# Kernel optimization log

Hardware: AMD Instinct MI355X
Metric: run time of the kernel (lower is better)

## Reference

```python
import jax, jax.numpy as jnp
import numpy as np

CROP_H = 7
CROP_W = 7
EXTRAP = 0.0  # module hardcodes 0 when calling CropAndResizeFunction


def _crop_and_resize(image, boxes, box_ind):
    """TF-style crop_and_resize.
    image: (N,C,H,W) float; boxes: (M,4) normalized (y1,x1,y2,x2); box_ind: (M,) int32.
    Returns (M,C,CROP_H,CROP_W).
    """
    N, C, H, W = image.shape
    dt = image.dtype
    y1, x1, y2, x2 = boxes[:, 0], boxes[:, 1], boxes[:, 2], boxes[:, 3]
    ii = jnp.arange(CROP_H, dtype=dt)
    jj = jnp.arange(CROP_W, dtype=dt)
    # sample coordinates in feature-map space, shape (M, CROP_H) / (M, CROP_W)
    y = y1[:, None] * (H - 1) + ii[None, :] * ((y2 - y1) * (H - 1) / (CROP_H - 1))[:, None]
    x = x1[:, None] * (W - 1) + jj[None, :] * ((x2 - x1) * (W - 1) / (CROP_W - 1))[:, None]
    valid_y = (y >= 0) & (y <= H - 1)
    valid_x = (x >= 0) & (x <= W - 1)
    yt_f = jnp.floor(y)
    xt_f = jnp.floor(x)
    y_lerp = y - yt_f  # (M, oh)
    x_lerp = x - xt_f  # (M, ow)
    yt = jnp.clip(yt_f, 0, H - 1).astype(jnp.int32)
    yb = jnp.clip(jnp.ceil(y), 0, H - 1).astype(jnp.int32)
    xl = jnp.clip(xt_f, 0, W - 1).astype(jnp.int32)
    xr = jnp.clip(jnp.ceil(x), 0, W - 1).astype(jnp.int32)
    img = jnp.transpose(image, (0, 2, 3, 1))  # (N,H,W,C) for clean gather
    b = box_ind[:, None, None]                # (M,1,1)
    tl = img[b, yt[:, :, None], xl[:, None, :]]  # (M,oh,ow,C)
    tr = img[b, yt[:, :, None], xr[:, None, :]]
    bl = img[b, yb[:, :, None], xl[:, None, :]]
    br = img[b, yb[:, :, None], xr[:, None, :]]
    xl_w = x_lerp[:, None, :, None]
    top = tl + (tr - tl) * xl_w
    bot = bl + (br - bl) * xl_w
    out = top + (bot - top) * y_lerp[:, :, None, None]
    valid = (valid_y[:, :, None] & valid_x[:, None, :])[..., None]
    out = jnp.where(valid, out, jnp.asarray(EXTRAP, dt))
    return jnp.transpose(out, (0, 3, 1, 2))  # (M,C,oh,ow)


def setup_inputs() -> dict:
    key = jax.random.key(0)
    k0, k1, k2, k3, k4, k5 = jax.random.split(key, 6)
    N, C, H, W = 2, 256, 200, 304
    M = 2048
    scale = 0.0625  # 1/16
    Himg, Wimg = H / scale, W / scale
    featuremap = jax.random.normal(k0, (N, C, H, W), dtype=jnp.float32)
    x1 = jax.random.uniform(k1, (M, 1), minval=0.0, maxval=Wimg - 260.0)
    y1 = jax.random.uniform(k2, (M, 1), minval=0.0, maxval=Himg - 260.0)
    bw = jax.random.uniform(k3, (M, 1), minval=32.0, maxval=256.0)
    bh = jax.random.uniform(k4, (M, 1), minval=32.0, maxval=256.0)
    ids = jax.random.randint(k5, (M, 1), 0, N).astype(jnp.float32)
    rois = jnp.concatenate([ids, x1, y1, x1 + bw, y1 + bh], axis=1)
    return {"featuremap": featuremap, "rois": rois, "spatial_scale": jnp.float32(scale)}


def reference(featuremap, rois, spatial_scale):
    H, W = featuremap.shape[2], featuremap.shape[3]
    boxes = rois[:, 1:5] * spatial_scale
    box_ind = rois[:, 0].astype(jnp.int32)
    x1, y1, x2, y2 = boxes[:, 0], boxes[:, 1], boxes[:, 2], boxes[:, 3]
    spacing_w = (x2 - x1) / CROP_W
    spacing_h = (y2 - y1) / CROP_H
    nx0 = (x1 + spacing_w / 2 - 0.5) / (W - 1)
    ny0 = (y1 + spacing_h / 2 - 0.5) / (H - 1)
    nw = spacing_w * (CROP_W - 1) / (W - 1)
    nh = spacing_h * (CROP_H - 1) / (H - 1)
    boxes_n = jnp.stack([ny0, nx0, ny0 + nh, nx0 + nw], axis=1)
    return _crop_and_resize(featuremap, boxes_n, box_ind)
```

## Files before the change

kernel.cpp:

```cpp
#include <hip/hip_runtime.h>

#define RA_C   256
#define RA_H   200
#define RA_W   304
#define RA_HW  (RA_H * RA_W)
#define RA_CHW (RA_C * RA_HW)
#define CROPN  7
#define CROP2  (CROPN * CROPN)
#define OUT_M  (RA_C * CROP2)
#define BC     8
#define BB     2
#define REG_R  16
#define REG_C  20
#define NF4    5
#define CH_STR (REG_R * REG_C + 4)
#define GREC   64

__global__ __launch_bounds__(256) void geom_kernel(
    const float* __restrict__ rois, const float* __restrict__ scale_p,
    int* __restrict__ ws, int M)
{
    const int gid = blockIdx.x * 256 + threadIdx.x;
    if (gid >= M * 2 * CROPN) return;
    {
        #pragma clang fp contract(off)
        const int m   = gid / (2 * CROPN);
        const int k14 = gid - m * (2 * CROPN);
        int* __restrict__ rec = ws + (size_t)m * GREC;
        const int axis = (k14 >= CROPN) ? 1 : 0;
        const int k = axis ? (k14 - CROPN) : k14;
        const float scale = scale_p[0];
        const float* __restrict__ rr = rois + (size_t)m * 5;
        float lo, hi, szm1;
        if (axis == 0) { lo = rr[2] * scale; hi = rr[4] * scale; szm1 = (float)(RA_H - 1); }
        else           { lo = rr[1] * scale; hi = rr[3] * scale; szm1 = (float)(RA_W - 1); }
        float sp   = (hi - lo) / 7.0f;
        float n0   = (lo + sp * 0.5f - 0.5f) / szm1;
        float nsz  = sp * 6.0f / szm1;
        float b2   = n0 + nsz;
        float d    = (b2 - n0) * szm1 / 6.0f;
        float coord = n0 * szm1 + (float)k * d;
        float fl = floorf(coord);
        float ce = ceilf(coord);
        float lerp = coord - fl;
        int lo_i = (int)fminf(fmaxf(fl, 0.0f), szm1);
        int hi_i = (int)fminf(fmaxf(ce, 0.0f), szm1);
        float valid = (coord >= 0.0f && coord <= szm1) ? 1.0f : 0.0f;
        if (axis == 0) {
            rec[k]      = lo_i;
            rec[7 + k]  = hi_i;
            rec[28 + k] = __float_as_int(lerp);
            rec[35 + k] = __float_as_int(valid);
            if (k == 0) {
                rec[56] = lo_i;
                rec[58] = (int)rr[0] * RA_CHW;
            }
        } else {
            rec[14 + k] = lo_i;
            rec[21 + k] = hi_i;
            rec[42 + k] = __float_as_int(lerp);
            rec[49 + k] = __float_as_int(valid);
            if (k == 0) rec[57] = lo_i & ~3;
        }
    }
}

__global__ __launch_bounds__(256) void roialign_kernel(
    const float* __restrict__ fm, const int* __restrict__ ws,
    float* __restrict__ out)
{
    __shared__ __align__(16) float s_reg[BB * BC * CH_STR];
    __shared__ int s_tab[BB][GREC];

    const int t = threadIdx.x;

    const int bid   = blockIdx.x;
    const int numBG = gridDim.x >> 5;
    const int xcd   = bid & 7;
    const int r     = bid >> 3;
    const int cgl   = r / numBG;
    const int bg    = r - cgl * numBG;
    const int m0    = bg * BB;
    const int c0    = (xcd * 4 + cgl) * BC;

    const int bx = t >> 7;
    const int* __restrict__ rec = ws + (size_t)(m0 + bx) * GREC;

    const int ys   = rec[56];
    const int xs   = rec[57];
    const int base = rec[58] + c0 * RA_HW;

    const int u   = t & 127;
    const int cc  = u >> 4;
    const int l16 = u & 15;
    const float* __restrict__ cp = fm + (size_t)(base + cc * RA_HW);
    float4 v[NF4];
    #pragma unroll
    for (int s = 0; s < NF4; ++s) {
        const int idx = l16 + (s << 4);
        const int r2  = idx / 5;
        const int kk  = idx - r2 * 5;
        const int row = min(ys + r2, RA_H - 1);
        const int col = min(xs + (kk << 2), RA_W - 4);
        v[s] = *reinterpret_cast<const float4*>(cp + row * RA_W + col);
    }

    if (t < BB * GREC) {
        const int b = t >> 6;
        const int w = t & 63;
        s_tab[b][w] = ws[(size_t)(m0 + b) * GREC + w];
    }

    {
        float* __restrict__ sp_ = s_reg + (bx * BC + cc) * CH_STR;
        #pragma unroll
        for (int s = 0; s < NF4; ++s) {
            const int idx = l16 + (s << 4);
            *reinterpret_cast<float4*>(sp_ + (idx << 2)) = v[s];
        }
    }
    __syncthreads();

    const int ij  = t & 63;
    const int chg = (t >> 6) & 1;
    if (ij < CROP2) {
        const int i = ij / CROPN;
        const int j = ij - i * CROPN;
        const int rT = min(s_tab[bx][i]      - ys, REG_R - 1);
        const int rB = min(s_tab[bx][7 + i]  - ys, REG_R - 1);
        const int cl = min(s_tab[bx][14 + j] - xs, REG_C - 1);
        const int cr = min(s_tab[bx][21 + j] - xs, REG_C - 1);
        const float yw = __int_as_float(s_tab[bx][28 + i]);
        const float vy = __int_as_float(s_tab[bx][35 + i]);
        const float xw = __int_as_float(s_tab[bx][42 + j]);
        const float vx = __int_as_float(s_tab[bx][49 + j]);
        const float vv = vy * vx;
        const int oT = rT * REG_C;
        const int oB = rB * REG_C;
        float* __restrict__ op =
            out + (size_t)(m0 + bx) * OUT_M + (size_t)(c0 + chg * 4) * CROP2 + ij;
        #pragma unroll
        for (int q = 0; q < 4; ++q) {
            const float* __restrict__ sp2 =
                s_reg + (bx * BC + chg * 4 + q) * CH_STR;
            const float tl = sp2[oT + cl];
            const float tr = sp2[oT + cr];
            const float bl = sp2[oB + cl];
            const float br = sp2[oB + cr];
            const float top = tl + (tr - tl) * xw;
            const float bot = bl + (br - bl) * xw;
            op[q * CROP2] = (top + (bot - top) * yw) * vv;
        }
    }
}

extern "C" void kernel_launch(void* const* d_in, const int* in_sizes, int n_in,
                              void* d_out, int out_size, void* d_ws, size_t ws_size,
                              hipStream_t stream) {
    const float* fm    = (const float*)d_in[0];
    const float* rois  = (const float*)d_in[1];
    const float* scale = (const float*)d_in[2];
    float* out = (float*)d_out;
    int* ws = (int*)d_ws;
    const int M = in_sizes[1] / 5;
    const int numBG = M / BB;

    const int gthreads = M * 2 * CROPN;
    geom_kernel<<<dim3((gthreads + 255) / 256), dim3(256), 0, stream>>>(
        rois, scale, ws, M);
    roialign_kernel<<<dim3(32 * numBG), dim3(256), 0, stream>>>(fm, ws, out);
}
```

Before: 273.6 us.

## Make roialign blocks persistent over four box pairs with register-prefetch pipelining

Each block now handles four consecutive box pairs instead of one. While interpolating the current pair from shared memory, it prefetches the next pair's feature-map region into registers and the geometry table into a double-buffered shared table. This cuts the grid by a factor of four and hides global-load latency behind the interpolation. The cost is two barriers per iteration, more register pressure, and fewer blocks to fill the GPU.

Result: slower. 423.8 us (+54.9%).

```diff
diff --git a/kernel.cpp b/kernel.cpp
--- a/kernel.cpp
+++ b/kernel.cpp
@@ -15,6 +15,8 @@
 #define NF4    5
 #define CH_STR (REG_R * REG_C + 4)
 #define GREC   64
+#define PREC   (BB * GREC)
+#define NITER  4
 
 __global__ __launch_bounds__(256) void geom_kernel(
     const float* __restrict__ rois, const float* __restrict__ scale_p,
@@ -70,48 +72,49 @@
     float* __restrict__ out)
 {
     __shared__ __align__(16) float s_reg[BB * BC * CH_STR];
-    __shared__ int s_tab[BB][GREC];
+    __shared__ int s_tab[2][PREC];
 
     const int t = threadIdx.x;
 
-    const int bid   = blockIdx.x;
-    const int numBG = gridDim.x >> 5;
-    const int xcd   = bid & 7;
-    const int r     = bid >> 3;
-    const int cgl   = r / numBG;
-    const int bg    = r - cgl * numBG;
-    const int m0    = bg * BB;
-    const int c0    = (xcd * 4 + cgl) * BC;
-
-    const int bx = t >> 7;
-    const int* __restrict__ rec = ws + (size_t)(m0 + bx) * GREC;
-
-    const int ys   = rec[56];
-    const int xs   = rec[57];
-    const int base = rec[58] + c0 * RA_HW;
-
+    const int bid    = blockIdx.x;
+    const int numBlk = gridDim.x >> 5;
+    const int xcd    = bid & 7;
+    const int r      = bid >> 3;
+    const int cgl    = r / numBlk;
+    const int bgrp   = r - cgl * numBlk;
+    const int c0     = (xcd * 4 + cgl) * BC;
+    const int mp0    = bgrp * NITER;
+
+    const int bx  = t >> 7;
     const int u   = t & 127;
     const int cc  = u >> 4;
     const int l16 = u & 15;
-    const float* __restrict__ cp = fm + (size_t)(base + cc * RA_HW);
-    float4 v[NF4];
-    #pragma unroll
-    for (int s = 0; s < NF4; ++s) {
-        const int idx = l16 + (s << 4);
-        const int r2  = idx / 5;
-        const int kk  = idx - r2 * 5;
-        const int row = min(ys + r2, RA_H - 1);
-        const int col = min(xs + (kk << 2), RA_W - 4);
-        v[s] = *reinterpret_cast<const float4*>(cp + row * RA_W + col);
-    }
-
-    if (t < BB * GREC) {
-        const int b = t >> 6;
-        const int w = t & 63;
-        s_tab[b][w] = ws[(size_t)(m0 + b) * GREC + w];
-    }
-
+
+    const int ij  = t & 63;
+    const int chg = (t >> 6) & 1;
+    const int si  = ij / CROPN;
+    const int sj  = ij - si * CROPN;
+
+    if (t < PREC) {
+        s_tab[0][t] = ws[(size_t)mp0 * PREC + t];
+        s_tab[1][t] = ws[(size_t)(mp0 + 1) * PREC + t];
+    }
     {
+        const int* __restrict__ rec0 = ws + (size_t)(mp0 * BB + bx) * GREC;
+        const int ys0   = rec0[56];
+        const int xs0   = rec0[57];
+        const int base0 = rec0[58] + c0 * RA_HW;
+        const float* __restrict__ cp0 = fm + (size_t)(base0 + cc * RA_HW);
+        float4 v[NF4];
+        #pragma unroll
+        for (int s = 0; s < NF4; ++s) {
+            const int idx = l16 + (s << 4);
+            const int r2  = idx / 5;
+            const int kk  = idx - r2 * 5;
+            const int row = min(ys0 + r2, RA_H - 1);
+            const int col = min(xs0 + (kk << 2), RA_W - 4);
+            v[s] = *reinterpret_cast<const float4*>(cp0 + row * RA_W + col);
+        }
         float* __restrict__ sp_ = s_reg + (bx * BC + cc) * CH_STR;
         #pragma unroll
         for (int s = 0; s < NF4; ++s) {
@@ -121,36 +124,76 @@
     }
     __syncthreads();
 
-    const int ij  = t & 63;
-    const int chg = (t >> 6) & 1;
-    if (ij < CROP2) {
-        const int i = ij / CROPN;
-        const int j = ij - i * CROPN;
-        const int rT = min(s_tab[bx][i]      - ys, REG_R - 1);
-        const int rB = min(s_tab[bx][7 + i]  - ys, REG_R - 1);
-        const int cl = min(s_tab[bx][14 + j] - xs, REG_C - 1);
-        const int cr = min(s_tab[bx][21 + j] - xs, REG_C - 1);
-        const float yw = __int_as_float(s_tab[bx][28 + i]);
-        const float vy = __int_as_float(s_tab[bx][35 + i]);
-        const float xw = __int_as_float(s_tab[bx][42 + j]);
-        const float vx = __int_as_float(s_tab[bx][49 + j]);
-        const float vv = vy * vx;
-        const int oT = rT * REG_C;
-        const int oB = rB * REG_C;
-        float* __restrict__ op =
-            out + (size_t)(m0 + bx) * OUT_M + (size_t)(c0 + chg * 4) * CROP2 + ij;
-        #pragma unroll
-        for (int q = 0; q < 4; ++q) {
-            const float* __restrict__ sp2 =
-                s_reg + (bx * BC + chg * 4 + q) * CH_STR;
-            const float tl = sp2[oT + cl];
-            const float tr = sp2[oT + cr];
-            const float bl = sp2[oB + cl];
-            const float br = sp2[oB + cr];
-            const float top = tl + (tr - tl) * xw;
-            const float bot = bl + (br - bl) * xw;
-            op[q * CROP2] = (top + (bot - top) * yw) * vv;
-        }
+    #pragma unroll
+    for (int it = 0; it < NITER; ++it) {
+        const int cur = it & 1;
+        const int nxt = cur ^ 1;
+
+        float4 vn[NF4];
+        if (it + 1 < NITER) {
+            const int* __restrict__ tbn = s_tab[nxt] + bx * GREC;
+            const int ysn   = tbn[56];
+            const int xsn   = tbn[57];
+            const int basen = tbn[58] + c0 * RA_HW;
+            const float* __restrict__ cpn = fm + (size_t)(basen + cc * RA_HW);
+            #pragma unroll
+            for (int s = 0; s < NF4; ++s) {
+                const int idx = l16 + (s << 4);
+                const int r2  = idx / 5;
+                const int kk  = idx - r2 * 5;
+                const int row = min(ysn + r2, RA_H - 1);
+                const int col = min(xsn + (kk << 2), RA_W - 4);
+                vn[s] = *reinterpret_cast<const float4*>(cpn + row * RA_W + col);
+            }
+        }
+        int rw = 0;
+        if (it + 2 < NITER && t < PREC)
+            rw = ws[(size_t)(mp0 + it + 2) * PREC + t];
+
+        if (ij < CROP2) {
+            const int* __restrict__ tb = s_tab[cur] + bx * GREC;
+            const int ysc = tb[56];
+            const int xsc = tb[57];
+            const int rT = min(tb[si]      - ysc, REG_R - 1);
+            const int rB = min(tb[7 + si]  - ysc, REG_R - 1);
+            const int cl = min(tb[14 + sj] - xsc, REG_C - 1);
+            const int cr = min(tb[21 + sj] - xsc, REG_C - 1);
+            const float yw = __int_as_float(tb[28 + si]);
+            const float vy = __int_as_float(tb[35 + si]);
+            const float xw = __int_as_float(tb[42 + sj]);
+            const float vx = __int_as_float(tb[49 + sj]);
+            const float vv = vy * vx;
+            const int oT = rT * REG_C;
+            const int oB = rB * REG_C;
+            const int m  = (mp0 + it) * BB + bx;
+            float* __restrict__ op =
+                out + (size_t)m * OUT_M + (size_t)(c0 + chg * 4) * CROP2 + ij;
+            #pragma unroll
+            for (int q = 0; q < 4; ++q) {
+                const float* __restrict__ sp2 =
+                    s_reg + (bx * BC + chg * 4 + q) * CH_STR;
+                const float tl = sp2[oT + cl];
+                const float tr = sp2[oT + cr];
+                const float bl = sp2[oB + cl];
+                const float br = sp2[oB + cr];
+                const float top = tl + (tr - tl) * xw;
+                const float bot = bl + (br - bl) * xw;
+                op[q * CROP2] = (top + (bot - top) * yw) * vv;
+            }
+        }
+        __syncthreads();
+
+        if (it + 1 < NITER) {
+            float* __restrict__ sp_ = s_reg + (bx * BC + cc) * CH_STR;
+            #pragma unroll
+            for (int s = 0; s < NF4; ++s) {
+                const int idx = l16 + (s << 4);
+                *reinterpret_cast<float4*>(sp_ + (idx << 2)) = vn[s];
+            }
+            if (it + 2 < NITER && t < PREC)
+                s_tab[cur][t] = rw;
+        }
+        __syncthreads();
     }
 }
 
@@ -163,10 +206,10 @@
     float* out = (float*)d_out;
     int* ws = (int*)d_ws;
     const int M = in_sizes[1] / 5;
-    const int numBG = M / BB;
+    const int numBlk = (M / BB) / NITER;
 
     const int gthreads = M * 2 * CROPN;
     geom_kernel<<<dim3((gthreads + 255) / 256), dim3(256), 0, stream>>>(
         rois, scale, ws, M);
-    roialign_kernel<<<dim3(32 * numBG), dim3(256), 0, stream>>>(fm, ws, out);
+    roialign_kernel<<<dim3(32 * numBlk), dim3(256), 0, stream>>>(fm, ws, out);
 }
```

## Sort ROIs by batch and spatial position before the gather kernel

Applied to the files above, without the earlier changes.

Adds a single-block bitonic sort kernel that orders ROI geometry records by (batch index, top row, left column) and copies them into a second workspace buffer. The gather kernel then processes spatially neighbouring ROIs in adjacent blocks and writes each result to the ROI's original output slot. The intent is better L2/MALL reuse of feature-map reads across overlapping ROIs. In exchange it adds an extra serial launch that runs on a single block, and the sorted path only runs when M is 2048 and the workspace is large enough.

New measurement: 348.9 us. 1.28x slower.

```diff
diff --git a/kernel.cpp b/kernel.cpp
--- a/kernel.cpp
+++ b/kernel.cpp
@@ -54,6 +54,7 @@
             if (k == 0) {
                 rec[56] = lo_i;
                 rec[58] = (int)rr[0] * RA_CHW;
+                rec[59] = m;
             }
         } else {
             rec[14 + k] = lo_i;
@@ -65,8 +66,43 @@
     }
 }
 
+__global__ __launch_bounds__(1024) void sort_kernel(int* __restrict__ ws, int M)
+{
+    __shared__ unsigned s_k[2048];
+    const int t = threadIdx.x;
+    for (int i = t; i < M; i += 1024) {
+        const int* __restrict__ rec = ws + (size_t)i * GREC;
+        const unsigned b  = rec[58] ? 1u : 0u;
+        const unsigned ys = (unsigned)rec[56] & 0xFFu;
+        const unsigned xs = (unsigned)rec[57] & 0x1FFu;
+        s_k[i] = (b << 28) | (ys << 20) | (xs << 11) | (unsigned)i;
+    }
+    __syncthreads();
+    for (unsigned k = 2; k <= 2048; k <<= 1) {
+        for (unsigned j = k >> 1; j > 0; j >>= 1) {
+            for (unsigned i = t; i < 2048; i += 1024) {
+                const unsigned ixj = i ^ j;
+                if (ixj > i) {
+                    const unsigned a = s_k[i], c = s_k[ixj];
+                    const bool descending = ((i & k) != 0);
+                    if ((a > c) != descending) { s_k[i] = c; s_k[ixj] = a; }
+                }
+            }
+            __syncthreads();
+        }
+    }
+    int* __restrict__ dst = ws + (size_t)M * GREC;
+    const int total = M * GREC;
+    for (int w = t; w < total; w += 1024) {
+        const int p    = w >> 6;
+        const int word = w & 63;
+        const int src  = (int)(s_k[p] & 0x7FFu);
+        dst[w] = ws[(size_t)src * GREC + word];
+    }
+}
+
 __global__ __launch_bounds__(256) void roialign_kernel(
-    const float* __restrict__ fm, const int* __restrict__ ws,
+    const float* __restrict__ fm, const int* __restrict__ recs,
     float* __restrict__ out)
 {
     __shared__ __align__(16) float s_reg[BB * BC * CH_STR];
@@ -84,7 +120,7 @@
     const int c0    = (xcd * 4 + cgl) * BC;
 
     const int bx = t >> 7;
-    const int* __restrict__ rec = ws + (size_t)(m0 + bx) * GREC;
+    const int* __restrict__ rec = recs + (size_t)(m0 + bx) * GREC;
 
     const int ys   = rec[56];
     const int xs   = rec[57];
@@ -108,7 +144,7 @@
     if (t < BB * GREC) {
         const int b = t >> 6;
         const int w = t & 63;
-        s_tab[b][w] = ws[(size_t)(m0 + b) * GREC + w];
+        s_tab[b][w] = recs[(size_t)(m0 + b) * GREC + w];
     }
 
     {
@@ -135,10 +171,11 @@
         const float xw = __int_as_float(s_tab[bx][42 + j]);
         const float vx = __int_as_float(s_tab[bx][49 + j]);
         const float vv = vy * vx;
+        const int am = s_tab[bx][59];
         const int oT = rT * REG_C;
         const int oB = rB * REG_C;
         float* __restrict__ op =
-            out + (size_t)(m0 + bx) * OUT_M + (size_t)(c0 + chg * 4) * CROP2 + ij;
+            out + (size_t)am * OUT_M + (size_t)(c0 + chg * 4) * CROP2 + ij;
         #pragma unroll
         for (int q = 0; q < 4; ++q) {
             const float* __restrict__ sp2 =
@@ -168,5 +205,12 @@
     const int gthreads = M * 2 * CROPN;
     geom_kernel<<<dim3((gthreads + 255) / 256), dim3(256), 0, stream>>>(
         rois, scale, ws, M);
-    roialign_kernel<<<dim3(32 * numBG), dim3(256), 0, stream>>>(fm, ws, out);
-}
+
+    const size_t need = (size_t)2 * M * GREC * sizeof(int);
+    const int* recs = ws;
+    if (ws_size >= need && M == 2048) {
+        sort_kernel<<<dim3(1), dim3(1024), 0, stream>>>(ws, M);
+        recs = ws + (size_t)M * GREC;
+    }
+    roialign_kernel<<<dim3(32 * numBG), dim3(256), 0, stream>>>(fm, recs, out);
+}
```
